# Kernel tuning notes

Hardware: AMD Instinct MI355X
Metric: run time of the kernel (lower is better)

Reference implementation:

```python
import jax, jax.numpy as jnp
import numpy as np
from functools import partial

EPS = 1e-12  # F.normalize eps (clamp_min on the norm)


def conv2d(x, w, b, groups=1):
    # x: [B, Cin, H, W], w: [Cout, Cin//groups, 3, 3], 'same' padding, stride 1
    y = jax.lax.conv_general_dilated(
        x, w, window_strides=(1, 1), padding='SAME',
        dimension_numbers=('NCHW', 'OIHW', 'NCHW'),
        feature_group_count=groups)
    return y + b[None, :, None, None]


def setup_inputs() -> dict:
    key = jax.random.key(0)
    ks = jax.random.split(key, 8)
    B, C, H, W = 16, 256, 32, 32
    HW = H * W
    T = 2  # tasks: seg, depth
    return {
        'features_seg': jax.random.normal(ks[0], (B, C, H, W), jnp.float32),
        'features_depth': jax.random.normal(ks[1], (B, C, H, W), jnp.float32),
        'proj_w_seg': jax.random.normal(ks[2], (C, C, 3, 3), jnp.float32) * 0.02,
        'proj_b_seg': jnp.zeros((C,), jnp.float32),
        'proj_w_depth': jax.random.normal(ks[3], (C, C, 3, 3), jnp.float32) * 0.02,
        'proj_b_depth': jnp.zeros((C,), jnp.float32),
        'fusion_w': jax.random.normal(ks[4], (HW, T, 3, 3), jnp.float32) * 0.02,
        'fusion_b': jnp.zeros((HW,), jnp.float32),
    }


def reference(features_seg, features_depth, proj_w_seg, proj_b_seg,
              proj_w_depth, proj_b_depth, fusion_w, fusion_b):
    gamma = 0.5
    feats = [features_seg, features_depth]
    proj = [(proj_w_seg, proj_b_seg), (proj_w_depth, proj_b_depth)]
    B, C, H, W = features_seg.shape
    HW = H * W

    # Per-task cosine-similarity affinity matrices [B, HW, HW]
    Ms = []
    for f in feats:
        fv = f.reshape(B, C, HW)
        fn = fv / jnp.maximum(jnp.linalg.norm(fv, axis=1, keepdims=True), EPS)
        aff = jnp.einsum('bci,bcj->bij', fn, fn)  # [B, HW, HW]
        Ms.append(aff.reshape(B, HW, H, W))

    # Stack on dim=2 then flatten -> interleaved channels [B, HW*T, H, W]
    M = jnp.stack(Ms, axis=2).reshape(B, -1, H, W)
    M = conv2d(M, fusion_w, fusion_b, groups=HW)  # [B, HW, H, W]

    attention = M.reshape(B, HW, HW).transpose(0, 2, 1)  # [B, HW, HW]

    outs = []
    for f, (w, b) in zip(feats, proj):
        value = conv2d(f, w, b).reshape(B, C, HW)          # [B, C, HW]
        attended = jnp.einsum('bck,bkj->bcj', value, attention)
        attended = attended.reshape(B, C, H, W)
        outs.append(gamma * attended + (1.0 - gamma) * f)
    return tuple(outs)
```

## Files before the change

kernel.cpp:

```cpp
#include <hip/hip_runtime.h>
#include <hip/hip_bf16.h>

typedef __bf16 bf16;
typedef __attribute__((ext_vector_type(8))) __bf16 bf16x8;
typedef __attribute__((ext_vector_type(4))) __bf16 bf16x4v;
typedef __attribute__((ext_vector_type(4))) float f32x4;

#define B_  16
#define C_  256
#define HW_ 1024
#define PADR 1156
#define ZSTR 295936
#define TP  133

__device__ __forceinline__ void gll16(const bf16* g, bf16* l) {
  __builtin_amdgcn_global_load_lds((const __attribute__((address_space(1))) void*)g,
                                   (__attribute__((address_space(3))) void*)l, 16, 0, 0);
}

__global__ void prep_fat(const float* __restrict__ f0, const float* __restrict__ f1,
                         const float* __restrict__ w0, const float* __restrict__ w1,
                         bf16* __restrict__ fTpad, float* __restrict__ rn,
                         bf16* __restrict__ Wr) {
  int tid = threadIdx.x;
  if (blockIdx.x >= 1024) {
    int i = (blockIdx.x - 1024) * 256 + tid;
    int t = i / 589824, r2 = i % 589824;
    int c = r2 / 2304, r = r2 % 2304;
    int cin = r / 9, d = r % 9;
    Wr[(size_t)t * 589824 + c * 2304 + d * 256 + cin] = (bf16)(t ? w1 : w0)[r2];
    return;
  }
  __shared__ float sm[256][33];
  __shared__ float ps[8][32];
  int bx = blockIdx.x & 31, z = blockIdx.x >> 5;
  int t = z >> 4, b = z & 15;
  int k0 = bx * 32;
  const float* fb = (t ? f1 : f0) + (size_t)b * C_ * HW_ + k0;
  int kk = tid & 31, cg = tid >> 5;
  float ssq = 0.f;
  #pragma unroll
  for (int i = 0; i < 32; ++i) {
    int c = cg + i * 8;
    float v = fb[(size_t)c * HW_ + kk];
    sm[c][kk] = v;
    ssq += v * v;
  }
  ps[cg][kk] = ssq;

  bf16x8 zv;
  #pragma unroll
  for (int e = 0; e < 8; ++e) zv[e] = (bf16)0.f;
  if (tid < 64) {
    int c = (tid & 31) * 8, side = tid >> 5;
    *(bf16x8*)(fTpad + ((size_t)z * PADR + (bx + 1) * 34 + side * 33) * C_ + c) = zv;
  }
  if (bx == 0 || bx == 31) {
    int prow = (bx == 0) ? 0 : 33;
    for (int q = tid; q < 34 * 32; q += 256) {
      int wcol = q >> 5, c = (q & 31) * 8;
      *(bf16x8*)(fTpad + ((size_t)z * PADR + prow * 34 + wcol) * C_ + c) = zv;
    }
  }

  __syncthreads();
  if (tid < 32) {
    float s = 0.f;
    #pragma unroll
    for (int r = 0; r < 8; ++r) s += ps[r][tid];
    rn[z * 1024 + k0 + tid] = 1.f / fmaxf(sqrtf(s), 1e-12f);
  }
  int wl = tid >> 3, c0 = (tid & 7) * 32;
  bf16* dst = fTpad + ((size_t)z * PADR + (bx + 1) * 34 + wl + 1) * C_ + c0;
  #pragma unroll
  for (int u = 0; u < 4; ++u) {
    bf16x8 vv;
    #pragma unroll
    for (int e = 0; e < 8; ++e) vv[e] = (bf16)sm[c0 + u * 8 + e][wl];
    *(bf16x8*)(dst + u * 8) = vv;
  }
}

__global__ void fusion_conv2(const bf16* __restrict__ aff, const float* __restrict__ fw,
                             const float* __restrict__ fb, bf16* __restrict__ M) {
  __shared__ float sa[2][1024];
  int bi = blockIdx.x;
  int i = bi & 1023, b = bi >> 10;
  int tid = threadIdx.x;
  #pragma unroll
  for (int t = 0; t < 2; ++t) {
    const bf16* arow = aff + (((size_t)t * 16 + b) * 1024 + i) * 1024;
    bf16x4v ch = ((const bf16x4v*)arow)[tid];
    sa[t][tid * 4 + 0] = (float)ch[0];
    sa[t][tid * 4 + 1] = (float)ch[1];
    sa[t][tid * 4 + 2] = (float)ch[2];
    sa[t][tid * 4 + 3] = (float)ch[3];
  }
  float wgt[2][9];
  #pragma unroll
  for (int t = 0; t < 2; ++t)
    #pragma unroll
    for (int q = 0; q < 9; ++q) wgt[t][q] = fw[i * 18 + t * 9 + q];
  float bias = fb[i];
  __syncthreads();
  #pragma unroll
  for (int s0 = 0; s0 < 4; ++s0) {
    int s = tid + s0 * 256;
    int h = s >> 5, w = s & 31;
    float acc = bias;
    #pragma unroll
    for (int kh = 0; kh < 3; ++kh) {
      int hh = h + kh - 1;
      if ((unsigned)hh < 32u) {
        #pragma unroll
        for (int kw = 0; kw < 3; ++kw) {
          int ww = w + kw - 1;
          if ((unsigned)ww < 32u) {
            acc += wgt[0][kh * 3 + kw] * sa[0][hh * 32 + ww];
            acc += wgt[1][kh * 3 + kw] * sa[1][hh * 32 + ww];
          }
        }
      }
    }
    M[((size_t)bi << 10) + s] = (bf16)acc;
  }
}

template<int MODE, int BM>
__device__ __forceinline__
void gemm_core(int bx, int by, int z, bf16* As, bf16* Bs, bf16* T,
               const bf16* __restrict__ A, long long sA,
               const bf16* __restrict__ Bm, long long sB, int K,
               bf16* __restrict__ Cb, long long sC,
               const float* __restrict__ x0, const float* __restrict__ x1,
               float* __restrict__ Co) {
  const int tt = (MODE == 1) ? (z >> 4) : (z & 1);
  const int bb = (MODE == 1) ? (z & 15) : (z >> 1);
  const int zold = tt * 16 + bb;
  const bf16* Ab = A + (size_t)(MODE == 3 ? tt : z) * sA;
  const bf16* Bb = Bm + (size_t)(MODE == 1 ? z : (MODE == 2 ? bb : zold)) * sB;
  const int m0 = by * BM, n0 = bx * 128;
  const int tid = threadIdx.x;
  const int lane = tid & 63, wave = tid >> 6;
  const int wm = (wave >> 1) * (BM / 2), wn = (wave & 1) * 64;
  const int fr = lane & 15, fq = lane >> 4;
  constexpr int MI = BM / 32;
  constexpr int SA = BM / 32;

  const bf16* srcA[SA];
  const bf16* srcB[4];
  int ldsA[SA], ldsB[4];
  #pragma unroll
  for (int s = 0; s < SA; ++s) {
    int q = (wave * SA + s) * 64 + lane;
    int row = q >> 3, c = (q & 7) ^ (row & 7);
    ldsA[s] = __builtin_amdgcn_readfirstlane((wave * SA + s) * 512);
    if (MODE == 1) {
      int j = m0 + row;
      srcA[s] = Ab + (size_t)(((j >> 5) + 1) * 34 + (j & 31) + 1) * C_ + c * 8;
    } else {
      srcA[s] = Ab + (size_t)(m0 + row) * K + c * 8;
    }
  }
  #pragma unroll
  for (int s = 0; s < 4; ++s) {
    int q = (wave * 4 + s) * 64 + lane;
    int row = q >> 3, c = (q & 7) ^ (row & 7);
    ldsB[s] = __builtin_amdgcn_readfirstlane((wave * 4 + s) * 512);
    int jb = n0 + row;
    if (MODE == 1 || MODE == 3) {
      srcB[s] = Bb + (size_t)(((jb >> 5) + 1) * 34 + (jb & 31) + 1) * C_ + c * 8;
    } else {
      srcB[s] = Bb + (size_t)jb * K + c * 8;
    }
  }
  int lA[2][MI], lB[2][4];
  #pragma unroll
  for (int h = 0; h < 2; ++h) {
    #pragma unroll
    for (int i = 0; i < MI; ++i) {
      int rr = wm + i * 16 + fr;
      lA[h][i] = rr * 64 + (((h * 4) + fq) ^ (rr & 7)) * 8;
    }
    #pragma unroll
    for (int j = 0; j < 4; ++j) {
      int rc = wn + j * 16 + fr;
      lB[h][j] = rc * 64 + (((h * 4) + fq) ^ (rc & 7)) * 8;
    }
  }

  f32x4 acc[MI][4];
  #pragma unroll
  for (int i = 0; i < MI; ++i)
    #pragma unroll
    for (int j = 0; j < 4; ++j) acc[i][j] = 0.f;

  for (int k0 = 0; k0 < K; k0 += 64) {
    int boff;
    if (MODE == 3) {
      int d = k0 >> 8;
      int kh = d / 3, kw = d % 3;
      boff = ((kh - 1) * 34 + (kw - 1)) * C_ + (k0 & 255);
    } else {
      boff = k0;
    }
    #pragma unroll
    for (int s = 0; s < SA; ++s) gll16(srcA[s] + k0, As + ldsA[s]);
    #pragma unroll
    for (int s = 0; s < 4; ++s) gll16(srcB[s] + boff, Bs + ldsB[s]);
    __syncthreads();
    #pragma unroll
    for (int h = 0; h < 2; ++h) {
      bf16x8 af[MI], bfr[4];
      #pragma unroll
      for (int i = 0; i < MI; ++i) af[i] = *(const bf16x8*)(&As[lA[h][i]]);
      #pragma unroll
      for (int j = 0; j < 4; ++j) bfr[j] = *(const bf16x8*)(&Bs[lB[h][j]]);
      #pragma unroll
      for (int i = 0; i < MI; ++i)
        #pragma unroll
        for (int j = 0; j < 4; ++j)
          acc[i][j] = __builtin_amdgcn_mfma_f32_16x16x32_bf16(af[i], bfr[j], acc[i][j], 0, 0, 0);
    }
    __syncthreads();
  }

  const bool mirror = (MODE == 1) && (bx != by);
  #pragma unroll
  for (int i = 0; i < MI; ++i) {
    int rbase = m0 + wm + i * 16 + fq * 4;
    #pragma unroll
    for (int j = 0; j < 4; ++j) {
      int col = n0 + wn + j * 16 + fr;
      float cj = (MODE == 1) ? x0[(size_t)z * 1024 + col] : 0.f;
      #pragma unroll
      for (int r = 0; r < 4; ++r) {
        int row = rbase + r;
        float v = acc[i][j][r];
        if (MODE == 1) {
          bf16 sv = (bf16)(v * x0[(size_t)z * 1024 + row] * cj);
          Cb[(size_t)z * sC + (size_t)row * 1024 + col] = sv;
          if (mirror) T[(row - m0) * TP + (col - n0)] = sv;
        } else if (MODE == 3) {
          const float* bias = tt ? x1 : x0;
          Cb[(size_t)z * sC + (size_t)row * 1024 + col] = (bf16)(v + bias[row]);
        } else {
          const float* fp = tt ? x1 : x0;
          Co[(size_t)zold * sC + (size_t)row * 1024 + col] =
              0.5f * v + 0.5f * fp[(size_t)bb * sC + (size_t)row * 1024 + col];
        }
      }
    }
  }
  if (mirror) {
    __syncthreads();
    #pragma unroll
    for (int s = 0; s < 8; ++s) {
      int q2 = s * 256 + tid;
      int g = q2 >> 4, c0 = (q2 & 15) << 3;
      bf16x8 vv;
      #pragma unroll
      for (int e = 0; e < 8; ++e) vv[e] = T[(c0 + e) * TP + g];
      *(bf16x8*)(Cb + (size_t)z * sC + (size_t)(n0 + g) * 1024 + m0 + c0) = vv;
    }
  }
}

__global__ __launch_bounds__(256, 4)
void gemm_aff(const bf16* __restrict__ fTpad, const float* __restrict__ rn,
              bf16* __restrict__ aff) {
  __shared__ bf16 smem[128 * TP];
  int q = blockIdx.x, by = 0, cnt = 8;
  while (q >= cnt) { q -= cnt; ++by; --cnt; }
  int bx = by + q;
  gemm_core<1, 128>(bx, by, blockIdx.z, smem, smem + 8192, smem,
                    fTpad, ZSTR, fTpad, ZSTR, C_,
                    aff, (long long)HW_ * HW_, rn, rn, nullptr);
}

__global__ __launch_bounds__(256, 4)
void gemm_value(const bf16* __restrict__ Wr, const bf16* __restrict__ fTpad,
                bf16* __restrict__ value, const float* __restrict__ b0,
                const float* __restrict__ b1) {
  __shared__ bf16 smem[64 * 64 + 128 * 64];
  gemm_core<3, 64>(blockIdx.x, blockIdx.y, blockIdx.z, smem, smem + 4096, nullptr,
                   Wr, 589824LL, fTpad, ZSTR, 2304,
                   value, (long long)C_ * HW_, b0, b1, nullptr);
}

__global__ __launch_bounds__(256, 4)
void gemm_attend(const bf16* __restrict__ value, const bf16* __restrict__ Mbuf,
                 const float* __restrict__ f0, const float* __restrict__ f1,
                 float* __restrict__ out) {
  __shared__ bf16 smem[64 * 64 + 128 * 64];
  gemm_core<2, 64>(blockIdx.x, blockIdx.y, blockIdx.z, smem, smem + 4096, nullptr,
                   value, (long long)C_ * HW_, Mbuf, (long long)HW_ * HW_, 1024,
                   nullptr, (long long)C_ * HW_, f0, f1, out);
}

extern "C" void kernel_launch(void* const* d_in, const int* in_sizes, int n_in,
                              void* d_out, int out_size, void* d_ws, size_t ws_size,
                              hipStream_t stream) {
  const float* f0 = (const float*)d_in[0];
  const float* f1 = (const float*)d_in[1];
  const float* w0 = (const float*)d_in[2];
  const float* b0 = (const float*)d_in[3];
  const float* w1 = (const float*)d_in[4];
  const float* b1 = (const float*)d_in[5];
  const float* fusion_w = (const float*)d_in[6];
  const float* fusion_b = (const float*)d_in[7];
  float* out = (float*)d_out;

  char* ws = (char*)d_ws;
  bf16* aff   = (bf16*)ws;
  bf16* Mbuf  = (bf16*)ws;
  bf16* fTpad = (bf16*)(ws + 67108864ull);
  bf16* Wr    = (bf16*)(ws + 86048768ull);
  bf16* value = (bf16*)(ws + 88408064ull);
  float* rn   = (float*)(ws + 105185280ull);

  prep_fat<<<5632, 256, 0, stream>>>(f0, f1, w0, w1, fTpad, rn, Wr);
  gemm_aff<<<dim3(36, 1, 32), 256, 0, stream>>>(fTpad, rn, aff);
  gemm_value<<<dim3(8, 4, 32), 256, 0, stream>>>(Wr, fTpad, value, b0, b1);
  fusion_conv2<<<16384, 256, 0, stream>>>(aff, fusion_w, fusion_b, Mbuf);
  gemm_attend<<<dim3(8, 4, 32), 256, 0, stream>>>(value, Mbuf, f0, f1, out);
}
```

Baseline: 240.3 us.

## Add triple-buffered 512-thread value-conv GEMM and enlarge attend GEMM tile

The value projection conv-GEMM is replaced by a dedicated 512-thread kernel. It computes a 256x128 tile per block and uses a three-stage LDS ring of async global-to-LDS loads with explicit vmcnt waits, plus s_setprio around the MFMA bursts, so loads overlap compute and the B tile is reused across all 256 output channels. The attend GEMM moves from 64-row to 128-row tiles, which halves its grid and raises operand reuse. In exchange, LDS use per block rises (about 144KB for the value kernel), which limits occupancy, and the manual waitcnt accounting must match the number of outstanding loads exactly.

```diff
diff --git a/kernel.cpp b/kernel.cpp
--- a/kernel.cpp
+++ b/kernel.cpp
@@ -137,8 +137,8 @@
   const int tt = (MODE == 1) ? (z >> 4) : (z & 1);
   const int bb = (MODE == 1) ? (z & 15) : (z >> 1);
   const int zold = tt * 16 + bb;
-  const bf16* Ab = A + (size_t)(MODE == 3 ? tt : z) * sA;
-  const bf16* Bb = Bm + (size_t)(MODE == 1 ? z : (MODE == 2 ? bb : zold)) * sB;
+  const bf16* Ab = A + (size_t)z * sA;
+  const bf16* Bb = Bm + (size_t)(MODE == 1 ? z : bb) * sB;
   const int m0 = by * BM, n0 = bx * 128;
   const int tid = threadIdx.x;
   const int lane = tid & 63, wave = tid >> 6;
@@ -168,7 +168,7 @@
     int row = q >> 3, c = (q & 7) ^ (row & 7);
     ldsB[s] = __builtin_amdgcn_readfirstlane((wave * 4 + s) * 512);
     int jb = n0 + row;
-    if (MODE == 1 || MODE == 3) {
+    if (MODE == 1) {
       srcB[s] = Bb + (size_t)(((jb >> 5) + 1) * 34 + (jb & 31) + 1) * C_ + c * 8;
     } else {
       srcB[s] = Bb + (size_t)jb * K + c * 8;
@@ -196,18 +196,10 @@
     for (int j = 0; j < 4; ++j) acc[i][j] = 0.f;
 
   for (int k0 = 0; k0 < K; k0 += 64) {
-    int boff;
-    if (MODE == 3) {
-      int d = k0 >> 8;
-      int kh = d / 3, kw = d % 3;
-      boff = ((kh - 1) * 34 + (kw - 1)) * C_ + (k0 & 255);
-    } else {
-      boff = k0;
-    }
     #pragma unroll
     for (int s = 0; s < SA; ++s) gll16(srcA[s] + k0, As + ldsA[s]);
     #pragma unroll
-    for (int s = 0; s < 4; ++s) gll16(srcB[s] + boff, Bs + ldsB[s]);
+    for (int s = 0; s < 4; ++s) gll16(srcB[s] + k0, Bs + ldsB[s]);
     __syncthreads();
     #pragma unroll
     for (int h = 0; h < 2; ++h) {
@@ -241,9 +233,6 @@
           bf16 sv = (bf16)(v * x0[(size_t)z * 1024 + row] * cj);
           Cb[(size_t)z * sC + (size_t)row * 1024 + col] = sv;
           if (mirror) T[(row - m0) * TP + (col - n0)] = sv;
-        } else if (MODE == 3) {
-          const float* bias = tt ? x1 : x0;
-          Cb[(size_t)z * sC + (size_t)row * 1024 + col] = (bf16)(v + bias[row]);
         } else {
           const float* fp = tt ? x1 : x0;
           Co[(size_t)zold * sC + (size_t)row * 1024 + col] =
@@ -279,23 +268,127 @@
 }
 
 __global__ __launch_bounds__(256, 4)
-void gemm_value(const bf16* __restrict__ Wr, const bf16* __restrict__ fTpad,
-                bf16* __restrict__ value, const float* __restrict__ b0,
-                const float* __restrict__ b1) {
-  __shared__ bf16 smem[64 * 64 + 128 * 64];
-  gemm_core<3, 64>(blockIdx.x, blockIdx.y, blockIdx.z, smem, smem + 4096, nullptr,
-                   Wr, 589824LL, fTpad, ZSTR, 2304,
-                   value, (long long)C_ * HW_, b0, b1, nullptr);
-}
-
-__global__ __launch_bounds__(256, 4)
 void gemm_attend(const bf16* __restrict__ value, const bf16* __restrict__ Mbuf,
                  const float* __restrict__ f0, const float* __restrict__ f1,
                  float* __restrict__ out) {
-  __shared__ bf16 smem[64 * 64 + 128 * 64];
-  gemm_core<2, 64>(blockIdx.x, blockIdx.y, blockIdx.z, smem, smem + 4096, nullptr,
-                   value, (long long)C_ * HW_, Mbuf, (long long)HW_ * HW_, 1024,
-                   nullptr, (long long)C_ * HW_, f0, f1, out);
+  __shared__ bf16 smem[128 * 128];
+  gemm_core<2, 128>(blockIdx.x, blockIdx.y, blockIdx.z, smem, smem + 8192, smem,
+                    value, (long long)C_ * HW_, Mbuf, (long long)HW_ * HW_, 1024,
+                    nullptr, (long long)C_ * HW_, f0, f1, out);
+}
+
+__global__ __launch_bounds__(512, 2)
+void gemm_value_p(const bf16* __restrict__ Wr, const bf16* __restrict__ fTpad,
+                  bf16* __restrict__ value, const float* __restrict__ b0,
+                  const float* __restrict__ b1) {
+  __shared__ bf16 smem3[3 * 24576];
+  const int z = blockIdx.y;
+  const int tt = z & 1, bb = z >> 1, zold = tt * 16 + bb;
+  const bf16* Ab = Wr + (size_t)tt * 589824;
+  const bf16* Bb = fTpad + (size_t)zold * ZSTR;
+  const int n0 = blockIdx.x * 128;
+  const int tid = threadIdx.x;
+  const int lane = tid & 63, wave = tid >> 6;
+  const int wm = (wave >> 1) * 64, wn = (wave & 1) * 64;
+  const int fr = lane & 15, fq = lane >> 4;
+
+  const bf16* srcA[4]; int ldsA[4];
+  #pragma unroll
+  for (int s = 0; s < 4; ++s) {
+    int q = s * 512 + tid;
+    int row = q >> 3, c = (q & 7) ^ (row & 7);
+    ldsA[s] = __builtin_amdgcn_readfirstlane(s * 4096 + wave * 512);
+    srcA[s] = Ab + (size_t)row * 2304 + c * 8;
+  }
+  const bf16* srcB[2]; int ldsB[2];
+  #pragma unroll
+  for (int s = 0; s < 2; ++s) {
+    int q = s * 512 + tid;
+    int row = q >> 3, c = (q & 7) ^ (row & 7);
+    ldsB[s] = __builtin_amdgcn_readfirstlane(s * 4096 + wave * 512);
+    int jb = n0 + row;
+    srcB[s] = Bb + (size_t)(((jb >> 5) + 1) * 34 + (jb & 31) + 1) * C_ + c * 8;
+  }
+
+  int lA[2][4], lB[2][4];
+  #pragma unroll
+  for (int h = 0; h < 2; ++h) {
+    #pragma unroll
+    for (int i = 0; i < 4; ++i) {
+      int rr = wm + i * 16 + fr;
+      lA[h][i] = rr * 64 + (((h * 4) + fq) ^ (rr & 7)) * 8;
+      int rc = wn + i * 16 + fr;
+      lB[h][i] = rc * 64 + (((h * 4) + fq) ^ (rc & 7)) * 8;
+    }
+  }
+
+  auto STAGE = [&](int t, int bufi) {
+    int k0 = t * 64;
+    int d = k0 >> 8;
+    int kh = d / 3, kw = d - kh * 3;
+    int boff = ((kh - 1) * 34 + (kw - 1)) * C_ + (k0 & 255);
+    bf16* As = smem3 + bufi * 24576;
+    bf16* Bs = As + 16384;
+    #pragma unroll
+    for (int s = 0; s < 4; ++s) gll16(srcA[s] + k0, As + ldsA[s]);
+    #pragma unroll
+    for (int s = 0; s < 2; ++s) gll16(srcB[s] + boff, Bs + ldsB[s]);
+  };
+
+  f32x4 acc[4][4];
+  #pragma unroll
+  for (int i = 0; i < 4; ++i)
+    #pragma unroll
+    for (int j = 0; j < 4; ++j) acc[i][j] = 0.f;
+
+  STAGE(0, 0);
+  STAGE(1, 1);
+
+  int cur = 0;
+  #pragma unroll 1
+  for (int t = 0; t < 36; ++t) {
+    if (t < 35) asm volatile("s_waitcnt vmcnt(6)" ::: "memory");
+    else        asm volatile("s_waitcnt vmcnt(0)" ::: "memory");
+    __builtin_amdgcn_s_barrier();
+    asm volatile("" ::: "memory");
+    if (t + 2 < 36) {
+      int nx = cur + 2; if (nx >= 3) nx -= 3;
+      STAGE(t + 2, nx);
+    }
+    bf16* As = smem3 + cur * 24576;
+    bf16* Bs = As + 16384;
+    #pragma unroll
+    for (int h = 0; h < 2; ++h) {
+      bf16x8 af[4], bv[4];
+      #pragma unroll
+      for (int i = 0; i < 4; ++i) af[i] = *(const bf16x8*)(As + lA[h][i]);
+      #pragma unroll
+      for (int j = 0; j < 4; ++j) bv[j] = *(const bf16x8*)(Bs + lB[h][j]);
+      __builtin_amdgcn_s_setprio(1);
+      #pragma unroll
+      for (int i = 0; i < 4; ++i)
+        #pragma unroll
+        for (int j = 0; j < 4; ++j)
+          acc[i][j] = __builtin_amdgcn_mfma_f32_16x16x32_bf16(af[i], bv[j], acc[i][j], 0, 0, 0);
+      __builtin_amdgcn_s_setprio(0);
+    }
+    ++cur; if (cur >= 3) cur = 0;
+  }
+
+  const float* bias = tt ? b1 : b0;
+  #pragma unroll
+  for (int i = 0; i < 4; ++i) {
+    #pragma unroll
+    for (int j = 0; j < 4; ++j) {
+      int col = n0 + wn + j * 16 + fr;
+      #pragma unroll
+      for (int r = 0; r < 4; ++r) {
+        int row = wm + i * 16 + fq * 4 + r;
+        value[(size_t)z * ((size_t)C_ * HW_) + (size_t)row * 1024 + col] =
+            (bf16)(acc[i][j][r] + bias[row]);
+      }
+    }
+  }
 }
 
 extern "C" void kernel_launch(void* const* d_in, const int* in_sizes, int n_in,
@@ -321,7 +414,7 @@
 
   prep_fat<<<5632, 256, 0, stream>>>(f0, f1, w0, w1, fTpad, rn, Wr);
   gemm_aff<<<dim3(36, 1, 32), 256, 0, stream>>>(fTpad, rn, aff);
-  gemm_value<<<dim3(8, 4, 32), 256, 0, stream>>>(Wr, fTpad, value, b0, b1);
+  gemm_value_p<<<dim3(8, 32), 512, 0, stream>>>(Wr, fTpad, value, b0, b1);
   fusion_conv2<<<16384, 256, 0, stream>>>(aff, fusion_w, fusion_b, Mbuf);
-  gemm_attend<<<dim3(8, 4, 32), 256, 0, stream>>>(value, Mbuf, f0, f1, out);
-}
+  gemm_attend<<<dim3(8, 2, 32), 256, 0, stream>>>(value, Mbuf, f0, f1, out);
+}
```

Result: faster. 233.4 us (-2.9%).
